# Performance work log

Measured on AMD Instinct MI355X. Metric: run time of the kernel, lower is better.

## Reference

```python
import jax, jax.numpy as jnp
import numpy as np

KERNEL_SIZE = 9   # temporal window Gamma (odd)
STRIDE = 1        # temporal stride; fifo_size = STRIDE*(K-1)+1
NUM_PARTITIONS = 3


def setup_inputs() -> dict:
    key = jax.random.key(0)
    k1, k2, k3, k4 = jax.random.split(key, 4)
    x = jax.random.normal(k1, (16, 64, 2048, 25), dtype=jnp.float32)         # (N, C_in, L, V)
    A = jax.random.uniform(k2, (3, 25, 25), dtype=jnp.float32)                # (P, V, V)
    conv_w = jax.random.normal(k3, (192, 64), dtype=jnp.float32) * 0.05       # (C_out*P, C_in) 1x1 conv
    conv_b = jax.random.normal(k4, (192,), dtype=jnp.float32) * 0.05
    return {"x": x, "A": A, "conv_w": conv_w, "conv_b": conv_b}


def reference(x, A, conv_w, conv_b):
    # x: (N, C_in, L, V); A: (P, V, V)
    N, C_in, L, V = x.shape
    P = A.shape[0]
    C_out = conv_w.shape[0] // P

    # residual: in_channels == out_channels and stride == 1 -> identity
    res = x

    # 1x1 conv over (L, V): pointwise channel mix
    a = jnp.einsum('nclv,oc->nolv', x, conv_w) + conv_b[None, :, None, None]  # (N, C_out*P, L, V)
    a = a.reshape(N, P, C_out, L, V)

    # per-partition adjacency matmul, summed over partitions (the FIFO loop
    # sums over partitions anyway, so the partition reduction fuses here)
    es = jnp.einsum('npclv,pvw->nlcw', a, A)  # (N, L, C_out, V)

    # FIFO windowed temporal sum: out[t] = sum_{k=0}^{K-1} es[t - k*STRIDE]
    # (frames before t=0 are zeros in the FIFO)
    pad = (KERNEL_SIZE - 1) * STRIDE
    padded = jnp.pad(es, ((0, 0), (pad, 0), (0, 0), (0, 0)))
    h = padded[:, 0:L]
    for j in range(1, KERNEL_SIZE):
        h = h + padded[:, j * STRIDE:j * STRIDE + L]
    h = jnp.transpose(h, (0, 2, 1, 3))  # (N, C_out, L, V)

    return jax.nn.relu(h + res)
```

## Files before the change

### kernel.cpp

```cpp
#include <hip/hip_runtime.h>

namespace {
constexpr int kL    = 2048;
constexpr int kV    = 25;
constexpr int kTL   = 8;
constexpr int kXsC  = kL * kV;
constexpr long kXsN = 64L * kXsC;

typedef __attribute__((ext_vector_type(8)))  short bf16x8;
typedef __attribute__((ext_vector_type(16))) float f32x16;
typedef __attribute__((ext_vector_type(4)))  unsigned short us4;

__device__ __forceinline__ float b2f(unsigned short u) {
  union { unsigned u32; float f; } x; x.u32 = ((unsigned)u) << 16; return x.f;
}
__device__ __forceinline__ unsigned short f2b(float f) {
  union { float f; unsigned u; } x; x.f = f;
  unsigned r = x.u + 0x7FFF + ((x.u >> 16) & 1);
  return (unsigned short)(r >> 16);
}
}

__global__ void stgcn_pre(const float* __restrict__ A,
                          const float* __restrict__ cw,
                          const float* __restrict__ cb,
                          unsigned short* __restrict__ wsu) {
  int tid = blockIdx.x * 256 + threadIdx.x;
  int nthr = gridDim.x * 256;
  for (int i = tid; i < 2 * 12 * 64 * 8; i += nthr) {
    int j = i & 7, lane = (i >> 3) & 63;
    int rem = i >> 9;
    int kg = rem % 12, mt2 = rem / 12;
    int c  = 32 * mt2 + (lane & 31);
    int p  = kg >> 2, ksl = kg & 3;
    int ci = 16 * ksl + 8 * (lane >> 5) + j;
    wsu[i] = f2b(cw[(p * 64 + c) * 64 + ci]);
  }
  for (int i = tid; i < 3 * 2 * 64 * 8; i += nthr) {
    int j = i & 7, lane = (i >> 3) & 63, ks = (i >> 9) & 1, p = i >> 10;
    int w = lane & 31;
    int v = 16 * ks + 8 * (lane >> 5) + j;
    float val = (v < kV && w < kV) ? A[(p * kV + v) * kV + w] : 0.f;
    wsu[12288 + i] = f2b(val);
  }
  float* bias2 = (float*)((char*)wsu + 30720);
  for (int i = tid; i < 64 * kV; i += nthr) {
    int c = i / kV, w = i % kV;
    float s = 0.f;
    for (int p = 0; p < 3; ++p) {
      float as = 0.f;
      for (int v = 0; v < kV; ++v) as += A[(p * kV + v) * kV + w];
      s += cb[p * 64 + c] * as;
    }
    bias2[i] = s;
  }
}

__global__ __launch_bounds__(512, 4)
void stgcn_main(const float* __restrict__ x,
                const unsigned short* __restrict__ wsu,
                float* __restrict__ out) {
  __shared__ unsigned short sBuf[34816];

  const int t    = threadIdx.x;
  const int lane = t & 63;
  const int wid  = t >> 6;
  const int hi   = lane >> 5;
  const int l31  = lane & 31;
  const int l0   = blockIdx.x * kTL;
  const float* xn = x + (long)blockIdx.y * kXsN;
  float* outn     = out + (long)blockIdx.y * kXsN;
  const float* bias2 = (const float*)((const char*)wsu + 30720);
  unsigned short* sRes = sBuf + 20480;

  {
    const int ci = t >> 3, q = t & 7;
    const int rowb = ci * 8 * 40;
    if (q == 7) {
      const int c4 = ((3 ^ (ci & 3)) << 3) | 4;
      us4 z = {0, 0, 0, 0};
      #pragma unroll
      for (int dl = 0; dl < 8; ++dl) *(us4*)&sBuf[rowb + dl * 40 + c4] = z;
    } else {
      const int colL = 4 * q;
      const int c4 = (((colL >> 3) ^ (ci & 3)) << 3) | (colL & 7);
      const float* xr = xn + (long)ci * kXsC + (long)(l0 - 8) * kV + colL;
      const int resb = ci * 8 * 28 + colL;
      const bool full = (q < 6);
      float a0 = 0.f, a1 = 0.f, a2 = 0.f, a3 = 0.f;
      if (l0) {
        #pragma unroll
        for (int j = 0; j < 8; ++j) {
          const float* r = xr + j * kV;
          a0 += r[0];
          if (full) { a1 += r[1]; a2 += r[2]; a3 += r[3]; }
        }
      }
      {
        const float* r = xr + 8 * kV;
        float x0 = r[0], x1 = full ? r[1] : 0.f, x2 = full ? r[2] : 0.f, x3 = full ? r[3] : 0.f;
        a0 += x0; a1 += x1; a2 += x2; a3 += x3;
        us4 rs = { f2b(x0), f2b(x1), f2b(x2), f2b(x3) };
        *(us4*)&sRes[resb] = rs;
      }
      #pragma unroll
      for (int dl = 0; dl < 8; ++dl) {
        us4 o = { f2b(a0), f2b(a1), f2b(a2), f2b(a3) };
        *(us4*)&sBuf[rowb + dl * 40 + c4] = o;
        if (dl < 7) {
          const float* pn = xr + (dl + 9) * kV;
          float x0 = pn[0], x1 = full ? pn[1] : 0.f, x2 = full ? pn[2] : 0.f, x3 = full ? pn[3] : 0.f;
          us4 rs = { f2b(x0), f2b(x1), f2b(x2), f2b(x3) };
          *(us4*)&sRes[resb + (dl + 1) * 28] = rs;
          a0 += x0; a1 += x1; a2 += x2; a3 += x3;
          if (l0) {
            const float* po = xr + dl * kV;
            a0 -= po[0];
            if (full) { a1 -= po[1]; a2 -= po[2]; a3 -= po[3]; }
          }
        }
      }
    }
  }
  __syncthreads();

  bf16x8 af[2][2];
  #pragma unroll
  for (int mtl = 0; mtl < 2; ++mtl) {
    const int m  = 32 * (2 * wid + mtl) + l31;
    const int cia = m >> 3;
    #pragma unroll
    for (int ks = 0; ks < 2; ++ks) {
      const int vblk = 2 * ks + hi;
      af[mtl][ks] = *(const bf16x8*)&sBuf[m * 40 + ((vblk ^ (cia & 3)) << 3)];
    }
  }
  __syncthreads();

  for (int i = t; i < 1536; i += 512) sBuf[12800 + i] = 0;

  const int mt2 = wid & 1;
  const int ng  = wid >> 1;
  const int nnt = (ng < 3) ? 2 : 1;
  const int nt0 = (ng < 3) ? 2 * ng : 6;

  f32x16 acc[2];
  #pragma unroll
  for (int q = 0; q < 2; ++q)
    #pragma unroll
    for (int r = 0; r < 16; ++r) acc[q][r] = 0.f;

  const bool wok = (l31 < kV);

  #define S1(p) {                                                             \
    _Pragma("unroll")                                                         \
    for (int mtl = 0; mtl < 2; ++mtl) {                                       \
      f32x16 cz;                                                              \
      _Pragma("unroll")                                                       \
      for (int r = 0; r < 16; ++r) cz[r] = 0.f;                               \
      _Pragma("unroll")                                                       \
      for (int ks = 0; ks < 2; ++ks) {                                        \
        bf16x8 bfr = *(const bf16x8*)&wsu[12288 + (((p) * 2 + ks) * 64 + lane) * 8]; \
        cz = __builtin_amdgcn_mfma_f32_32x32x16_bf16(af[mtl][ks], bfr, cz, 0, 0, 0); \
      }                                                                       \
      if (wok) {                                                              \
        _Pragma("unroll")                                                     \
        for (int r = 0; r < 16; ++r) {                                        \
          const int mo = (r & 3) + 8 * (r >> 2) + 4 * hi;                     \
          const int m  = 32 * (2 * wid + mtl) + mo;                           \
          const int ci = m >> 3;                                              \
          const int nidx = (m & 7) * kV + l31;                                \
          sBuf[nidx * 64 + (((ci >> 3) ^ (nidx & 7)) << 3) + (ci & 7)] = f2b(cz[r]); \
        }                                                                     \
      }                                                                       \
    }                                                                         \
  }

  #define S2(p) {                                                             \
    _Pragma("unroll")                                                         \
    for (int ksl = 0; ksl < 4; ++ksl) {                                       \
      bf16x8 wf = *(const bf16x8*)&wsu[((mt2 * 12 + (p) * 4 + ksl) * 64 + lane) * 8]; \
      _Pragma("unroll")                                                       \
      for (int q = 0; q < 2; ++q) {                                           \
        if (q < nnt) {                                                        \
          const int nidx = 32 * (nt0 + q) + l31;                              \
          const int o = 2 * ksl + hi;                                         \
          bf16x8 yf = *(const bf16x8*)&sBuf[nidx * 64 + ((o ^ (nidx & 7)) << 3)]; \
          acc[q] = __builtin_amdgcn_mfma_f32_32x32x16_bf16(wf, yf, acc[q], 0, 0, 0); \
        }                                                                     \
      }                                                                       \
    }                                                                         \
  }

  S1(0); __syncthreads();
  S2(0); __syncthreads();
  S1(1); __syncthreads();
  S2(1); __syncthreads();
  S1(2); __syncthreads();
  S2(2);

  #undef S1
  #undef S2

  #pragma unroll
  for (int q = 0; q < 2; ++q) {
    if (q < nnt) {
      const int nidx = 32 * (nt0 + q) + l31;
      if (nidx < 200) {
        const int dl = nidx / 25, wv = nidx - 25 * (nidx / 25);
        const float cnt = l0 ? 9.f : (float)(dl + 1);
        const long base = (long)(l0 + dl) * kV + wv;
        #pragma unroll
        for (int r = 0; r < 16; ++r) {
          const int c = 32 * mt2 + (r & 3) + 8 * (r >> 2) + 4 * hi;
          float val = acc[q][r] + cnt * bias2[c * kV + wv]
                    + b2f(sRes[(c * 8 + dl) * 28 + wv]);
          outn[(long)c * kXsC + base] = fmaxf(val, 0.f);
        }
      }
    }
  }
}

extern "C" void kernel_launch(void* const* d_in, const int* in_sizes, int n_in,
                              void* d_out, int out_size, void* d_ws, size_t ws_size,
                              hipStream_t stream) {
  const float* x  = (const float*)d_in[0];
  const float* A  = (const float*)d_in[1];
  const float* cw = (const float*)d_in[2];
  const float* cb = (const float*)d_in[3];
  unsigned short* wsu = (unsigned short*)d_ws;

  hipLaunchKernelGGL(stgcn_pre, dim3(8), dim3(256), 0, stream, A, cw, cb, wsu);
  hipLaunchKernelGGL(stgcn_main, dim3(kL / kTL, 16), dim3(512), 0, stream,
                     x, wsu, (float*)d_out);
}
```

Measured before the change: 256.3 us.

## Use hardware bf16 pack conversion, remap block order, drop padding zero-fill

```diff
diff --git a/kernel.cpp b/kernel.cpp
--- a/kernel.cpp
+++ b/kernel.cpp
@@ -18,6 +18,11 @@
   union { float f; unsigned u; } x; x.f = f;
   unsigned r = x.u + 0x7FFF + ((x.u >> 16) & 1);
   return (unsigned short)(r >> 16);
+}
+__device__ __forceinline__ unsigned cvt_pk(float lo, float hi) {
+  unsigned r;
+  asm("v_cvt_pk_bf16_f32 %0, %1, %2" : "=v"(r) : "v"(lo), "v"(hi));
+  return r;
 }
 }
 
@@ -67,9 +72,15 @@
   const int wid  = t >> 6;
   const int hi   = lane >> 5;
   const int l31  = lane & 31;
-  const int l0   = blockIdx.x * kTL;
-  const float* xn = x + (long)blockIdx.y * kXsN;
-  float* outn     = out + (long)blockIdx.y * kXsN;
+
+  const int b   = blockIdx.x + (int)gridDim.x * blockIdx.y;
+  const int w_  = (b & 7) * 512 + (b >> 3);
+  const int lt  = w_ & 255;
+  const int nb  = w_ >> 8;
+  const int l0  = lt * kTL;
+
+  const float* xn = x + (long)nb * kXsN;
+  float* outn     = out + (long)nb * kXsN;
   const float* bias2 = (const float*)((const char*)wsu + 30720);
   unsigned short* sRes = sBuf + 20480;
 
@@ -78,9 +89,9 @@
     const int rowb = ci * 8 * 40;
     if (q == 7) {
       const int c4 = ((3 ^ (ci & 3)) << 3) | 4;
-      us4 z = {0, 0, 0, 0};
+      uint2 z = {0u, 0u};
       #pragma unroll
-      for (int dl = 0; dl < 8; ++dl) *(us4*)&sBuf[rowb + dl * 40 + c4] = z;
+      for (int dl = 0; dl < 8; ++dl) *(uint2*)&sBuf[rowb + dl * 40 + c4] = z;
     } else {
       const int colL = 4 * q;
       const int c4 = (((colL >> 3) ^ (ci & 3)) << 3) | (colL & 7);
@@ -100,18 +111,18 @@
         const float* r = xr + 8 * kV;
         float x0 = r[0], x1 = full ? r[1] : 0.f, x2 = full ? r[2] : 0.f, x3 = full ? r[3] : 0.f;
         a0 += x0; a1 += x1; a2 += x2; a3 += x3;
-        us4 rs = { f2b(x0), f2b(x1), f2b(x2), f2b(x3) };
-        *(us4*)&sRes[resb] = rs;
+        uint2 rs = { cvt_pk(x0, x1), cvt_pk(x2, x3) };
+        *(uint2*)&sRes[resb] = rs;
       }
       #pragma unroll
       for (int dl = 0; dl < 8; ++dl) {
-        us4 o = { f2b(a0), f2b(a1), f2b(a2), f2b(a3) };
-        *(us4*)&sBuf[rowb + dl * 40 + c4] = o;
+        uint2 o = { cvt_pk(a0, a1), cvt_pk(a2, a3) };
+        *(uint2*)&sBuf[rowb + dl * 40 + c4] = o;
         if (dl < 7) {
           const float* pn = xr + (dl + 9) * kV;
           float x0 = pn[0], x1 = full ? pn[1] : 0.f, x2 = full ? pn[2] : 0.f, x3 = full ? pn[3] : 0.f;
-          us4 rs = { f2b(x0), f2b(x1), f2b(x2), f2b(x3) };
-          *(us4*)&sRes[resb + (dl + 1) * 28] = rs;
+          uint2 rs = { cvt_pk(x0, x1), cvt_pk(x2, x3) };
+          *(uint2*)&sRes[resb + (dl + 1) * 28] = rs;
           a0 += x0; a1 += x1; a2 += x2; a3 += x3;
           if (l0) {
             const float* po = xr + dl * kV;
@@ -137,7 +148,6 @@
   }
   __syncthreads();
 
-  for (int i = t; i < 1536; i += 512) sBuf[12800 + i] = 0;
 
   const int mt2 = wid & 1;
   const int ng  = wid >> 1;
@@ -170,7 +180,8 @@
           const int m  = 32 * (2 * wid + mtl) + mo;                           \
           const int ci = m >> 3;                                              \
           const int nidx = (m & 7) * kV + l31;                                \
-          sBuf[nidx * 64 + (((ci >> 3) ^ (nidx & 7)) << 3) + (ci & 7)] = f2b(cz[r]); \
+          sBuf[nidx * 64 + (((ci >> 3) ^ (nidx & 7)) << 3) + (ci & 7)] =      \
+              (unsigned short)cvt_pk(cz[r], cz[r]);                           \
         }                                                                     \
       }                                                                       \
     }                                                                         \
```

Measured after the change: 238.3 us. 7.0% less time.
